# Kernel optimization log

Hardware: AMD Instinct MI355X
Metric: run time of the kernel (lower is better)

## Reference

```python
import jax, jax.numpy as jnp
import numpy as np

Q_DIM = 9   # state(7) + action(2)
KV_DIM = 5  # fixed by get_input_tensors: 4 relative features + r_trans
H = 3
D = KV_DIM * H  # 15


def setup_inputs() -> dict:
    key = jax.random.key(0)
    ks = jax.random.split(key, 16)
    b, t = 32, 256

    def u(k, shape, fan_in):
        lim = (1.0 / fan_in) ** 0.5
        return jax.random.uniform(k, shape, jnp.float32, -lim, lim)

    return {
        "state": jax.random.normal(ks[0], (b, t, 7), jnp.float32),
        "action": jax.random.normal(ks[1], (b, t, 2), jnp.float32),
        "Wk": u(ks[2], (D, KV_DIM), KV_DIM),
        "Wq": u(ks[3], (D, Q_DIM), Q_DIM),
        "Wv": u(ks[4], (D, KV_DIM), KV_DIM),
        "att_bias": jax.random.uniform(ks[5], (KV_DIM,), jnp.float32, -0.1, 0.1),
        "Wscore": u(ks[6], (1, KV_DIM), KV_DIM),
        "bscore": u(ks[7], (1,), KV_DIM),
        "g1": jnp.ones((D,), jnp.float32),
        "beta1": jnp.zeros((D,), jnp.float32),
        "W1": u(ks[8], (5 * D, D), D),
        "bff1": u(ks[9], (5 * D,), D),
        "W2": u(ks[10], (D, 5 * D), 5 * D),
        "bff2": u(ks[11], (D,), 5 * D),
        "g2": jnp.ones((D,), jnp.float32),
        "beta2": jnp.zeros((D,), jnp.float32),
    }


def _layernorm(x, g, b, eps=1e-5):
    m = jnp.mean(x, axis=-1, keepdims=True)
    v = jnp.var(x, axis=-1, keepdims=True)
    return (x - m) * jax.lax.rsqrt(v + eps) * g + b


def _get_input_tensors(state):
    b, t, _ = state.shape
    init = state[..., :4]                                  # (b,t,4)
    rel = init[:, None, :, :] - init[:, :, None, :]        # (b,t,t,4): row i, col j -> s_j - s_i
    xy = rel.reshape(b, t, t, 2, 2).transpose(0, 1, 2, 4, 3)  # [...,0,:]=(x,vx), [...,1,:]=(y,vy)
    ang = -state[..., -1] + 0.5 * jnp.pi                   # (b,t)
    c = jnp.cos(ang)[:, None, :, None]                     # broadcast over row dim -> angle of col j
    s = jnp.sin(ang)[:, None, :, None]
    xr = xy[..., 0, :] * c - xy[..., 1, :] * s             # (b,t,t,2)
    yr = xy[..., 0, :] * s + xy[..., 1, :] * c
    rel = jnp.concatenate([xr, yr], axis=3)                # [xn,vxn,yn,vyn]
    rel = rel.reshape(b, t, t, 2, 2).transpose(0, 1, 2, 4, 3).reshape(b, t, t, 4)  # [xn,yn,vxn,vyn]
    # drop diagonal (j != i) via precomputed off-diagonal column indices
    rows = jnp.arange(t)[:, None]
    j = jnp.arange(t - 1)[None, :]
    cols = j + (j >= rows)                                 # (t,t-1)
    rel = rel[:, rows, cols, :]                            # (b,t,t-1,4)
    r = jnp.sqrt(rel[..., 0] ** 2 + rel[..., 1] ** 2)[..., None]  # (b,t,t-1,1)
    r_trans = 1.0 / (1.0 + jnp.exp(-1.0 + 5.0 * (r - 0.2)))
    kv_x = jnp.concatenate([rel[..., :2] / r, rel[..., 2:], r_trans], axis=-1)  # (b,t,t-1,5)
    return state, kv_x


def reference(state, action, Wk, Wq, Wv, att_bias, Wscore, bscore,
              g1, beta1, W1, bff1, W2, bff2, g2, beta2):
    q_x, kv_x = _get_input_tensors(state)
    q_x = jnp.concatenate([q_x, action], axis=-1)          # (b,t,Q_DIM)
    b, t, tm1, _ = kv_x.shape

    keys = (kv_x @ Wk.T).reshape(b, t, tm1, H, KV_DIM)     # (b,t,t-1,h,k)
    queries = (q_x @ Wq.T).reshape(b, t, 1, H, KV_DIM)
    e = jnp.tanh(keys + queries + att_bias)
    score = (e @ Wscore.T + bscore)[..., 0]                # (b,t,t-1,h)
    values = (kv_x @ Wv.T).reshape(b, t, tm1, H, KV_DIM)
    w = jax.nn.softmax(score, axis=2)                      # softmax over the t-1 neighbours
    x = jnp.einsum('btjh,btjhk->bthk', w, values).reshape(b, t, H * KV_DIM)

    x = _layernorm(x, g1, beta1)
    y = jax.nn.relu(x @ W1.T + bff1) @ W2.T + bff2
    x = x + y
    return _layernorm(x, g2, beta2)
```

## Files before the change

### kernel.cpp

```cpp
#include <hip/hip_runtime.h>
#include <math.h>

#define TT   256
#define TM1  255
#define QD   9
#define KD   5
#define NH   3
#define DD   15
#define HID  75
#define NR   18

__device__ __forceinline__ float fast_rcp(float x) {
    return __builtin_amdgcn_rcpf(x);
}

template<int CTRL>
__device__ __forceinline__ float dpp_add(float x) {
    int y = __builtin_amdgcn_update_dpp(0, __float_as_int(x), CTRL, 0xf, 0xf, true);
    return x + __int_as_float(y);
}

__device__ __forceinline__ float wave_sum63(float x) {
    x = dpp_add<0x111>(x);
    x = dpp_add<0x112>(x);
    x = dpp_add<0x114>(x);
    x = dpp_add<0x118>(x);
    x = dpp_add<0x142>(x);
    x = dpp_add<0x143>(x);
    return x;
}

__device__ __forceinline__ float bcast(float x, int l) {
    return __int_as_float(__builtin_amdgcn_readlane(__float_as_int(x), l));
}

__global__ __launch_bounds__(64)
void fused_block_kernel(const float* __restrict__ state,
                        const float* __restrict__ action,
                        const float* __restrict__ Wk,
                        const float* __restrict__ Wq,
                        const float* __restrict__ Wv,
                        const float* __restrict__ att_bias,
                        const float* __restrict__ Wscore,
                        const float* __restrict__ bscore,
                        const float* __restrict__ g1,
                        const float* __restrict__ beta1,
                        const float* __restrict__ W1,
                        const float* __restrict__ bff1,
                        const float* __restrict__ W2,
                        const float* __restrict__ bff2,
                        const float* __restrict__ g2,
                        const float* __restrict__ beta2,
                        float* __restrict__ out)
{
    const int blk = blockIdx.x;
    const int b   = blk >> 8;
    const int qi  = blk & 255;
    const int m   = threadIdx.x;

    __shared__ __align__(16) float s_h[76];

    const float* sti = state + ((size_t)b*TT + qi)*7;
    const float si0 = sti[0], si1 = sti[1], si2 = sti[2], si3 = sti[3];

    float qv = 0.0f;
    if (m < DD) {
        float acc = att_bias[m % KD];
        #pragma unroll
        for (int k = 0; k < 7; k++) acc = fmaf(Wq[m*QD+k], sti[k], acc);
        acc = fmaf(Wq[m*QD+7], action[((size_t)b*TT+qi)*2 + 0], acc);
        acc = fmaf(Wq[m*QD+8], action[((size_t)b*TT+qi)*2 + 1], acc);
        qv = acc;
    }
    float qb[DD];
    #pragma unroll
    for (int d = 0; d < DD; d++) qb[d] = bcast(qv, d);

    float wsc2[KD];
    float C = bscore[0];
    #pragma unroll
    for (int kk = 0; kk < KD; kk++) { float w = Wscore[kk]; wsc2[kk] = -2.0f*w; C += w; }

    float red[NR];
    #pragma unroll
    for (int n = 0; n < NR; n++) red[n] = 0.0f;

    #pragma unroll
    for (int pp = 0; pp < 4; pp++) {
        const int mm = m + pp*64;
        if (mm < TM1) {
            const int jj = mm + (mm >= qi ? 1 : 0);
            const float* stj = state + ((size_t)b*TT + jj)*7;
            const float d0 = stj[0]-si0, d1 = stj[1]-si1;
            const float d2 = stj[2]-si2, d3 = stj[3]-si3;
            float cs, sn;
            __sincosf(stj[6], &cs, &sn);
            const float xr0 = d0*cs - d1*sn, yr0 = d0*sn + d1*cs;
            const float xr1 = d2*cs - d3*sn, yr1 = d2*sn + d3*cs;
            const float s2   = xr0*xr0 + yr0*yr0;
            const float rinv = __builtin_amdgcn_rsqf(s2);
            const float r    = s2 * rinv;
            const float rt   = fast_rcp(1.0f + __expf(fmaf(5.0f, r, -2.0f)));
            const float kv0 = xr0*rinv, kv1 = yr0*rinv;

            #pragma unroll
            for (int h = 0; h < NH; h++) {
                float sc = C;
                #pragma unroll
                for (int kk = 0; kk < KD; kk++) {
                    const int d = h*KD + kk;
                    float a = qb[d];
                    a = fmaf(Wk[d*KD+0], kv0, a);
                    a = fmaf(Wk[d*KD+1], kv1, a);
                    a = fmaf(Wk[d*KD+2], xr1, a);
                    a = fmaf(Wk[d*KD+3], yr1, a);
                    a = fmaf(Wk[d*KD+4], rt , a);
                    sc = fmaf(wsc2[kk], fast_rcp(__expf(a + a) + 1.0f), sc);
                }
                const float p = __expf(sc);
                red[h] += p;
                red[NH+h*KD+0] = fmaf(p, kv0, red[NH+h*KD+0]);
                red[NH+h*KD+1] = fmaf(p, kv1, red[NH+h*KD+1]);
                red[NH+h*KD+2] = fmaf(p, xr1, red[NH+h*KD+2]);
                red[NH+h*KD+3] = fmaf(p, yr1, red[NH+h*KD+3]);
                red[NH+h*KD+4] = fmaf(p, rt , red[NH+h*KD+4]);
            }
        }
    }

    #pragma unroll
    for (int n = 0; n < NR; n++) red[n] = wave_sum63(red[n]);
    float fin[NR];
    #pragma unroll
    for (int n = 0; n < NR; n++) fin[n] = bcast(red[n], 63);

    float xm = 0.0f;
    if (m < DD) {
        const int h = m / KD;
        float acc = 0.0f;
        #pragma unroll
        for (int c = 0; c < KD; c++) acc = fmaf(Wv[m*KD+c], fin[NH+h*KD+c], acc);
        xm = acc * fast_rcp(fin[h]);
    }

    float s1 = xm, sq = xm*xm;
    #pragma unroll
    for (int off = 8; off >= 1; off >>= 1) {
        s1 += __shfl_xor(s1, off, 16);
        sq += __shfl_xor(sq, off, 16);
    }
    const float mu1   = s1 * (1.0f/DD);
    const float rstd1 = rsqrtf(sq * (1.0f/DD) - mu1*mu1 + 1e-5f);
    float xln = 0.0f;
    if (m < DD) xln = (xm - mu1) * rstd1 * g1[m] + beta1[m];

    float xs[DD];
    #pragma unroll
    for (int d = 0; d < DD; d++) xs[d] = bcast(xln, d);

    {
        float h0 = bff1[m];
        #pragma unroll
        for (int k = 0; k < DD; k++) h0 = fmaf(W1[m*DD+k], xs[k], h0);
        s_h[m] = fmaxf(h0, 0.0f);
        if (m < HID-64) {
            float h1 = bff1[m+64];
            #pragma unroll
            for (int k = 0; k < DD; k++) h1 = fmaf(W1[(m+64)*DD+k], xs[k], h1);
            s_h[m+64] = fmaxf(h1, 0.0f);
        }
        if (m == 11) s_h[75] = 0.0f;
    }
    __syncthreads();

    float x2 = 0.0f;
    if (m < DD) {
        float acc = bff2[m];
        const float4* hv = (const float4*)s_h;
        #pragma unroll
        for (int c = 0; c < 18; c++) {
            const float4 hh = hv[c];
            acc = fmaf(W2[m*HID + 4*c+0], hh.x, acc);
            acc = fmaf(W2[m*HID + 4*c+1], hh.y, acc);
            acc = fmaf(W2[m*HID + 4*c+2], hh.z, acc);
            acc = fmaf(W2[m*HID + 4*c+3], hh.w, acc);
        }
        acc = fmaf(W2[m*HID+72], s_h[72], acc);
        acc = fmaf(W2[m*HID+73], s_h[73], acc);
        acc = fmaf(W2[m*HID+74], s_h[74], acc);
        x2 = xln + acc;
    }
    float t1 = x2, t2 = x2*x2;
    #pragma unroll
    for (int off = 8; off >= 1; off >>= 1) {
        t1 += __shfl_xor(t1, off, 16);
        t2 += __shfl_xor(t2, off, 16);
    }
    const float mu2   = t1 * (1.0f/DD);
    const float rstd2 = rsqrtf(t2 * (1.0f/DD) - mu2*mu2 + 1e-5f);
    if (m < DD)
        out[(size_t)blk*DD + m] = (x2 - mu2) * rstd2 * g2[m] + beta2[m];
}

extern "C" void kernel_launch(void* const* d_in, const int* in_sizes, int n_in,
                              void* d_out, int out_size, void* d_ws, size_t ws_size,
                              hipStream_t stream) {
    const float* state    = (const float*)d_in[0];
    const float* action   = (const float*)d_in[1];
    const float* Wk       = (const float*)d_in[2];
    const float* Wq       = (const float*)d_in[3];
    const float* Wv       = (const float*)d_in[4];
    const float* att_bias = (const float*)d_in[5];
    const float* Wscore   = (const float*)d_in[6];
    const float* bscore   = (const float*)d_in[7];
    const float* g1       = (const float*)d_in[8];
    const float* beta1    = (const float*)d_in[9];
    const float* W1       = (const float*)d_in[10];
    const float* bff1     = (const float*)d_in[11];
    const float* W2       = (const float*)d_in[12];
    const float* bff2     = (const float*)d_in[13];
    const float* g2       = (const float*)d_in[14];
    const float* beta2    = (const float*)d_in[15];
    float* out = (float*)d_out;

    dim3 grid(32 * 256);
    dim3 block(64);
    fused_block_kernel<<<grid, block, 0, stream>>>(
        state, action, Wk, Wq, Wv, att_bias, Wscore, bscore,
        g1, beta1, W1, bff1, W2, bff2, g2, beta2, out);
}
```

Before: 29.66 us.

## Prefetch neighbour rows, mask attention tail branchlessly, split W2 matvec across lanes

The neighbour state row for the next iteration is loaded one step ahead in registers, so global-load latency overlaps the tanh/exp attention math. The `mm < TM1` branch becomes a score offset of -100, so every lane runs the same path with no divergence. The W2 matvec is split across three 16-lane groups that each handle 25 hidden units, then combined with shuffles, so it no longer runs serially on 15 lanes. It also swaps sin and cos to match the reference rotation angle, clamps the squared radius to avoid division by zero, and adds an occupancy hint of 8 to launch_bounds, which may limit registers.

After: 31.41 us. +5.9%, slower.

```diff
diff --git a/kernel.cpp b/kernel.cpp
--- a/kernel.cpp
+++ b/kernel.cpp
@@ -34,7 +34,7 @@
     return __int_as_float(__builtin_amdgcn_readlane(__float_as_int(x), l));
 }
 
-__global__ __launch_bounds__(64)
+__global__ __launch_bounds__(64, 8)
 void fused_block_kernel(const float* __restrict__ state,
                         const float* __restrict__ action,
                         const float* __restrict__ Wk,
@@ -58,9 +58,10 @@
     const int qi  = blk & 255;
     const int m   = threadIdx.x;
 
-    __shared__ __align__(16) float s_h[76];
-
-    const float* sti = state + ((size_t)b*TT + qi)*7;
+    __shared__ __align__(16) float s_h[HID];
+
+    const float* __restrict__ sb  = state + (size_t)b*TT*7;
+    const float* __restrict__ sti = sb + qi*7;
     const float si0 = sti[0], si1 = sti[1], si2 = sti[2], si3 = sti[3];
 
     float qv = 0.0f;
@@ -85,46 +86,62 @@
     #pragma unroll
     for (int n = 0; n < NR; n++) red[n] = 0.0f;
 
+    float nrow[7];
+    {
+        const int j0 = m + (m >= qi ? 1 : 0);
+        #pragma unroll
+        for (int k = 0; k < 7; k++) nrow[k] = sb[j0*7 + k];
+    }
+
     #pragma unroll
     for (int pp = 0; pp < 4; pp++) {
-        const int mm = m + pp*64;
-        if (mm < TM1) {
-            const int jj = mm + (mm >= qi ? 1 : 0);
-            const float* stj = state + ((size_t)b*TT + jj)*7;
-            const float d0 = stj[0]-si0, d1 = stj[1]-si1;
-            const float d2 = stj[2]-si2, d3 = stj[3]-si3;
-            float cs, sn;
-            __sincosf(stj[6], &cs, &sn);
-            const float xr0 = d0*cs - d1*sn, yr0 = d0*sn + d1*cs;
-            const float xr1 = d2*cs - d3*sn, yr1 = d2*sn + d3*cs;
-            const float s2   = xr0*xr0 + yr0*yr0;
-            const float rinv = __builtin_amdgcn_rsqf(s2);
-            const float r    = s2 * rinv;
-            const float rt   = fast_rcp(1.0f + __expf(fmaf(5.0f, r, -2.0f)));
-            const float kv0 = xr0*rinv, kv1 = yr0*rinv;
-
+        float crow[7];
+        #pragma unroll
+        for (int k = 0; k < 7; k++) crow[k] = nrow[k];
+        if (pp < 3) {
+            const int mmn = m + (pp+1)*64;
+            int jn = mmn + (mmn >= qi ? 1 : 0);
+            jn = (jn <= TM1) ? jn : TM1;
             #pragma unroll
-            for (int h = 0; h < NH; h++) {
-                float sc = C;
-                #pragma unroll
-                for (int kk = 0; kk < KD; kk++) {
-                    const int d = h*KD + kk;
-                    float a = qb[d];
-                    a = fmaf(Wk[d*KD+0], kv0, a);
-                    a = fmaf(Wk[d*KD+1], kv1, a);
-                    a = fmaf(Wk[d*KD+2], xr1, a);
-                    a = fmaf(Wk[d*KD+3], yr1, a);
-                    a = fmaf(Wk[d*KD+4], rt , a);
-                    sc = fmaf(wsc2[kk], fast_rcp(__expf(a + a) + 1.0f), sc);
-                }
-                const float p = __expf(sc);
-                red[h] += p;
-                red[NH+h*KD+0] = fmaf(p, kv0, red[NH+h*KD+0]);
-                red[NH+h*KD+1] = fmaf(p, kv1, red[NH+h*KD+1]);
-                red[NH+h*KD+2] = fmaf(p, xr1, red[NH+h*KD+2]);
-                red[NH+h*KD+3] = fmaf(p, yr1, red[NH+h*KD+3]);
-                red[NH+h*KD+4] = fmaf(p, rt , red[NH+h*KD+4]);
+            for (int k = 0; k < 7; k++) nrow[k] = sb[jn*7 + k];
+        }
+        const int   mm = m + pp*64;
+        const float Cp = (mm < TM1) ? C : -100.0f;
+
+        const float d0 = crow[0]-si0, d1 = crow[1]-si1;
+        const float d2 = crow[2]-si2, d3 = crow[3]-si3;
+        const float th = crow[6];
+        const float cs = __sinf(th);
+        const float sn = __cosf(th);
+        const float xr0 = d0*cs - d1*sn, yr0 = d0*sn + d1*cs;
+        const float xr1 = d2*cs - d3*sn, yr1 = d2*sn + d3*cs;
+        const float s2   = fmaxf(fmaf(xr0, xr0, yr0*yr0), 1e-12f);
+        const float rinv = __builtin_amdgcn_rsqf(s2);
+        const float r    = s2 * rinv;
+        const float rt   = fast_rcp(1.0f + __expf(fmaf(5.0f, r, -2.0f)));
+        const float kv0 = xr0*rinv, kv1 = yr0*rinv;
+
+        #pragma unroll
+        for (int h = 0; h < NH; h++) {
+            float sc = Cp;
+            #pragma unroll
+            for (int kk = 0; kk < KD; kk++) {
+                const int d = h*KD + kk;
+                float a = qb[d];
+                a = fmaf(Wk[d*KD+0], kv0, a);
+                a = fmaf(Wk[d*KD+1], kv1, a);
+                a = fmaf(Wk[d*KD+2], xr1, a);
+                a = fmaf(Wk[d*KD+3], yr1, a);
+                a = fmaf(Wk[d*KD+4], rt , a);
+                sc = fmaf(wsc2[kk], fast_rcp(__expf(a + a) + 1.0f), sc);
             }
+            const float p = __expf(sc);
+            red[h] += p;
+            red[NH+h*KD+0] = fmaf(p, kv0, red[NH+h*KD+0]);
+            red[NH+h*KD+1] = fmaf(p, kv1, red[NH+h*KD+1]);
+            red[NH+h*KD+2] = fmaf(p, xr1, red[NH+h*KD+2]);
+            red[NH+h*KD+3] = fmaf(p, yr1, red[NH+h*KD+3]);
+            red[NH+h*KD+4] = fmaf(p, rt , red[NH+h*KD+4]);
         }
     }
 
@@ -169,27 +186,23 @@
             for (int k = 0; k < DD; k++) h1 = fmaf(W1[(m+64)*DD+k], xs[k], h1);
             s_h[m+64] = fmaxf(h1, 0.0f);
         }
-        if (m == 11) s_h[75] = 0.0f;
     }
     __syncthreads();
 
+    const int c2 = m >> 4;
+    const int d2 = m & 15;
+    const int cc = (c2 < 3) ? c2 : 2;
+    const int dc = (d2 < DD) ? d2 : 0;
+    float acc2 = 0.0f;
+    #pragma unroll
+    for (int k = 0; k < 25; k++)
+        acc2 = fmaf(W2[dc*HID + cc*25 + k], s_h[cc*25 + k], acc2);
+    acc2 = (c2 < 3) ? acc2 : 0.0f;
+    acc2 += __shfl_xor(acc2, 16);
+    acc2 += __shfl_xor(acc2, 32);
+
     float x2 = 0.0f;
-    if (m < DD) {
-        float acc = bff2[m];
-        const float4* hv = (const float4*)s_h;
-        #pragma unroll
-        for (int c = 0; c < 18; c++) {
-            const float4 hh = hv[c];
-            acc = fmaf(W2[m*HID + 4*c+0], hh.x, acc);
-            acc = fmaf(W2[m*HID + 4*c+1], hh.y, acc);
-            acc = fmaf(W2[m*HID + 4*c+2], hh.z, acc);
-            acc = fmaf(W2[m*HID + 4*c+3], hh.w, acc);
-        }
-        acc = fmaf(W2[m*HID+72], s_h[72], acc);
-        acc = fmaf(W2[m*HID+73], s_h[73], acc);
-        acc = fmaf(W2[m*HID+74], s_h[74], acc);
-        x2 = xln + acc;
-    }
+    if (m < DD) x2 = xln + bff2[m] + acc2;
     float t1 = x2, t2 = x2*x2;
     #pragma unroll
     for (int off = 8; off >= 1; off >>= 1) {
```
